# Optimization experiments

Measured on AMD Instinct MI355X. Metric: run time of the kernel, lower is better.

The kernel has to match this reference:

```python
import jax, jax.numpy as jnp
import numpy as np

RANK = 8
ALPHA = 16.0
SCALING = ALPHA / RANK
EPS = 1e-8


def setup_inputs() -> dict:
    key = jax.random.key(0)
    k1, k2, k3, k4 = jax.random.split(key, 4)
    B, S, D_IN, D_OUT = 4, 2048, 4096, 4096
    x = jax.random.normal(k1, (B, S, D_IN), dtype=jnp.float32)
    base_output = jax.random.normal(k2, (B, S, D_OUT), dtype=jnp.float32)
    base_weight = jax.random.normal(k3, (D_OUT, D_IN), dtype=jnp.float32) * 0.02
    # orthogonal init for lora_A (rank x in_features)
    g = jax.random.normal(k4, (D_IN, RANK), dtype=jnp.float32)
    q, _ = jnp.linalg.qr(g)
    lora_A = q.T.astype(jnp.float32)  # [rank, in]
    # lora_B initialized to zeros in the module; use small random values so
    # the delta path is numerically exercised.
    lora_B = jax.random.normal(jax.random.fold_in(key, 5), (D_OUT, RANK), dtype=jnp.float32) * 0.01
    magnitude = jnp.ones((D_OUT,), dtype=jnp.float32)
    return {
        "x": x,
        "base_output": base_output,
        "base_weight": base_weight,
        "lora_A": lora_A,
        "lora_B": lora_B,
        "magnitude": magnitude,
    }


def reference(x, base_output, base_weight, lora_A, lora_B, magnitude):
    # Low-rank path: x @ A^T @ B^T, scaled.  (dropout p=0 -> identity)
    lora_x = jnp.einsum("bsi,ri->bsr", x, lora_A)            # [B,S,r]
    lora_out = jnp.einsum("bsr,or->bso", lora_x, lora_B)     # [B,S,out]
    delta_v = lora_out * SCALING
    # DoRA-style row norm of the updated weight (materializes full delta,
    # matching the original math exactly).
    updated_weight = base_weight + (lora_B @ lora_A) * SCALING  # [out,in]
    updated_norm = jnp.linalg.norm(updated_weight, axis=1) + EPS  # [out]
    mag_scale = magnitude / updated_norm                          # [out]
    output = (base_output + delta_v) * mag_scale[None, None, :]
    return output
```

## Files before the change

kernel.cpp:

```cpp
#include <hip/hip_runtime.h>
#include <math.h>

#define D_IN   4096
#define D_OUT  4096
#define M_ROWS 8192
#define RANK   8
#define SCALING 2.0f
#define EPS_N  1e-8f

__global__ __launch_bounds__(256) void k_magscale(
    const float* __restrict__ W,
    const float* __restrict__ A,
    const float* __restrict__ Bl,
    const float* __restrict__ mag,
    float* __restrict__ mag_scale,
    float* __restrict__ Bm)
{
    const int wave = threadIdx.x >> 6;
    const int lane = threadIdx.x & 63;
    const int o = blockIdx.x * 4 + wave;
    const float* Wrow = W + (size_t)o * D_IN;

    float b[RANK];
#pragma unroll
    for (int r = 0; r < RANK; ++r) b[r] = Bl[o * RANK + r];

    float acc = 0.f;
    for (int i = lane * 4; i < D_IN; i += 64 * 4) {
        float4 w4 = *(const float4*)(Wrow + i);
        float dx = 0.f, dy = 0.f, dz = 0.f, dw = 0.f;
#pragma unroll
        for (int r = 0; r < RANK; ++r) {
            float4 a4 = *(const float4*)(A + r * D_IN + i);
            dx += b[r] * a4.x; dy += b[r] * a4.y;
            dz += b[r] * a4.z; dw += b[r] * a4.w;
        }
        float tx = w4.x + SCALING * dx;
        float ty = w4.y + SCALING * dy;
        float tz = w4.z + SCALING * dz;
        float tw = w4.w + SCALING * dw;
        acc += tx * tx + ty * ty + tz * tz + tw * tw;
    }
#pragma unroll
    for (int off = 32; off > 0; off >>= 1)
        acc += __shfl_down(acc, off, 64);

    if (lane == 0) {
        float ms = mag[o] / (sqrtf(acc) + EPS_N);
        mag_scale[o] = ms;
#pragma unroll
        for (int r = 0; r < RANK; ++r)
            Bm[o * RANK + r] = SCALING * b[r] * ms;
    }
}

__global__ __launch_bounds__(256) void k_lorax(
    const float* __restrict__ x,
    const float* __restrict__ A,
    float* __restrict__ lx)
{
    const int wave = threadIdx.x >> 6;
    const int lane = threadIdx.x & 63;
    const int m = blockIdx.x * 4 + wave;
    const float* xrow = x + (size_t)m * D_IN;

    float acc[RANK] = {};
    for (int i = lane * 4; i < D_IN; i += 64 * 4) {
        float4 x4 = *(const float4*)(xrow + i);
#pragma unroll
        for (int r = 0; r < RANK; ++r) {
            float4 a4 = *(const float4*)(A + r * D_IN + i);
            acc[r] += x4.x * a4.x + x4.y * a4.y + x4.z * a4.z + x4.w * a4.w;
        }
    }
#pragma unroll
    for (int r = 0; r < RANK; ++r) {
#pragma unroll
        for (int off = 32; off > 0; off >>= 1)
            acc[r] += __shfl_down(acc[r], off, 64);
    }
    if (lane == 0) {
#pragma unroll
        for (int r = 0; r < RANK; ++r)
            lx[m * RANK + r] = acc[r];
    }
}

#define MT 16
#define OT 1024

__global__ __launch_bounds__(256) void k_out(
    const float* __restrict__ base,
    const float* __restrict__ lx,
    const float* __restrict__ Bm,
    const float* __restrict__ mag_scale,
    float* __restrict__ out)
{
    const int ob = (blockIdx.x & (D_OUT / OT - 1)) * OT;
    const int mb = (blockIdx.x / (D_OUT / OT)) * MT;
    const int o = ob + threadIdx.x * 4;

    float ms[4];
    float bm[4][RANK];
#pragma unroll
    for (int j = 0; j < 4; ++j) {
        ms[j] = mag_scale[o + j];
#pragma unroll
        for (int r = 0; r < RANK; ++r)
            bm[j][r] = Bm[(size_t)(o + j) * RANK + r];
    }

    __shared__ float slx[MT][RANK];
    if (threadIdx.x < MT * RANK) {
        int mi = threadIdx.x / RANK, r = threadIdx.x % RANK;
        slx[mi][r] = lx[(size_t)(mb + mi) * RANK + r];
    }
    __syncthreads();

    for (int mi = 0; mi < MT; ++mi) {
        const size_t row = (size_t)(mb + mi) * D_OUT + o;
        float4 b4 = *(const float4*)(base + row);
        float l[RANK];
#pragma unroll
        for (int r = 0; r < RANK; ++r) l[r] = slx[mi][r];

        float rx = b4.x * ms[0];
        float ry = b4.y * ms[1];
        float rz = b4.z * ms[2];
        float rw = b4.w * ms[3];
#pragma unroll
        for (int r = 0; r < RANK; ++r) {
            rx += l[r] * bm[0][r];
            ry += l[r] * bm[1][r];
            rz += l[r] * bm[2][r];
            rw += l[r] * bm[3][r];
        }
        float4 o4 = make_float4(rx, ry, rz, rw);
        *(float4*)(out + row) = o4;
    }
}

extern "C" void kernel_launch(void* const* d_in, const int* in_sizes, int n_in,
                              void* d_out, int out_size, void* d_ws, size_t ws_size,
                              hipStream_t stream) {
    const float* x        = (const float*)d_in[0];
    const float* base_out = (const float*)d_in[1];
    const float* base_w   = (const float*)d_in[2];
    const float* lora_A   = (const float*)d_in[3];
    const float* lora_B   = (const float*)d_in[4];
    const float* mag      = (const float*)d_in[5];
    float* out = (float*)d_out;

    float* mag_scale = (float*)d_ws;
    float* Bm        = mag_scale + D_OUT;
    float* lx        = Bm + (size_t)D_OUT * RANK;

    k_magscale<<<D_OUT / 4, 256, 0, stream>>>(base_w, lora_A, lora_B, mag,
                                              mag_scale, Bm);
    k_lorax<<<M_ROWS / 4, 256, 0, stream>>>(x, lora_A, lx);
    k_out<<<(M_ROWS / MT) * (D_OUT / OT), 256, 0, stream>>>(base_out, lx, Bm,
                                                            mag_scale, out);
}
```

Baseline: 439.1 us.

## Fuse LoRA projection into output kernel and process two weight rows per wave

Merges the x·A^T projection kernel into the output kernel. Each block computes lora_x for 16 rows into shared memory and then writes all 4096 output columns for those rows, which removes one launch and the lx round trip through global memory. Each wave now handles 4 x rows and the magnitude kernel handles 2 weight rows per wave, so each load of A is reused across more rows. The cost is fewer blocks (512) with larger per-thread register use, which may limit occupancy and memory-level parallelism on the large streaming passes.

```diff
diff --git a/kernel.cpp b/kernel.cpp
--- a/kernel.cpp
+++ b/kernel.cpp
@@ -8,7 +8,7 @@
 #define SCALING 2.0f
 #define EPS_N  1e-8f
 
-__global__ __launch_bounds__(256) void k_magscale(
+__global__ __launch_bounds__(256, 2) void k_magscale(
     const float* __restrict__ W,
     const float* __restrict__ A,
     const float* __restrict__ Bl,
@@ -18,125 +18,145 @@
 {
     const int wave = threadIdx.x >> 6;
     const int lane = threadIdx.x & 63;
-    const int o = blockIdx.x * 4 + wave;
-    const float* Wrow = W + (size_t)o * D_IN;
+    const int o0 = blockIdx.x * 8 + wave * 2;
+    const float* W0 = W + (size_t)o0 * D_IN;
+    const float* W1 = W0 + D_IN;
 
-    float b[RANK];
+    float b0[RANK], b1[RANK];
 #pragma unroll
-    for (int r = 0; r < RANK; ++r) b[r] = Bl[o * RANK + r];
+    for (int r = 0; r < RANK; ++r) {
+        b0[r] = Bl[o0 * RANK + r];
+        b1[r] = Bl[(o0 + 1) * RANK + r];
+    }
 
-    float acc = 0.f;
-    for (int i = lane * 4; i < D_IN; i += 64 * 4) {
-        float4 w4 = *(const float4*)(Wrow + i);
-        float dx = 0.f, dy = 0.f, dz = 0.f, dw = 0.f;
+    float acc0 = 0.f, acc1 = 0.f;
+    for (int i = lane * 4; i < D_IN; i += 256) {
+        float4 a4[RANK];
+#pragma unroll
+        for (int r = 0; r < RANK; ++r)
+            a4[r] = *(const float4*)(A + r * D_IN + i);
+        float4 w0 = *(const float4*)(W0 + i);
+        float4 w1 = *(const float4*)(W1 + i);
+
+        float d0x = 0.f, d0y = 0.f, d0z = 0.f, d0w = 0.f;
+        float d1x = 0.f, d1y = 0.f, d1z = 0.f, d1w = 0.f;
 #pragma unroll
         for (int r = 0; r < RANK; ++r) {
-            float4 a4 = *(const float4*)(A + r * D_IN + i);
-            dx += b[r] * a4.x; dy += b[r] * a4.y;
-            dz += b[r] * a4.z; dw += b[r] * a4.w;
+            d0x += b0[r] * a4[r].x; d0y += b0[r] * a4[r].y;
+            d0z += b0[r] * a4[r].z; d0w += b0[r] * a4[r].w;
+            d1x += b1[r] * a4[r].x; d1y += b1[r] * a4[r].y;
+            d1z += b1[r] * a4[r].z; d1w += b1[r] * a4[r].w;
         }
-        float tx = w4.x + SCALING * dx;
-        float ty = w4.y + SCALING * dy;
-        float tz = w4.z + SCALING * dz;
-        float tw = w4.w + SCALING * dw;
-        acc += tx * tx + ty * ty + tz * tz + tw * tw;
+        float t;
+        t = w0.x + SCALING * d0x; acc0 += t * t;
+        t = w0.y + SCALING * d0y; acc0 += t * t;
+        t = w0.z + SCALING * d0z; acc0 += t * t;
+        t = w0.w + SCALING * d0w; acc0 += t * t;
+        t = w1.x + SCALING * d1x; acc1 += t * t;
+        t = w1.y + SCALING * d1y; acc1 += t * t;
+        t = w1.z + SCALING * d1z; acc1 += t * t;
+        t = w1.w + SCALING * d1w; acc1 += t * t;
     }
 #pragma unroll
-    for (int off = 32; off > 0; off >>= 1)
-        acc += __shfl_down(acc, off, 64);
-
+    for (int off = 32; off > 0; off >>= 1) {
+        acc0 += __shfl_down(acc0, off, 64);
+        acc1 += __shfl_down(acc1, off, 64);
+    }
     if (lane == 0) {
-        float ms = mag[o] / (sqrtf(acc) + EPS_N);
-        mag_scale[o] = ms;
-#pragma unroll
-        for (int r = 0; r < RANK; ++r)
-            Bm[o * RANK + r] = SCALING * b[r] * ms;
-    }
-}
-
-__global__ __launch_bounds__(256) void k_lorax(
-    const float* __restrict__ x,
-    const float* __restrict__ A,
-    float* __restrict__ lx)
-{
-    const int wave = threadIdx.x >> 6;
-    const int lane = threadIdx.x & 63;
-    const int m = blockIdx.x * 4 + wave;
-    const float* xrow = x + (size_t)m * D_IN;
-
-    float acc[RANK] = {};
-    for (int i = lane * 4; i < D_IN; i += 64 * 4) {
-        float4 x4 = *(const float4*)(xrow + i);
+        float ms0 = mag[o0] / (sqrtf(acc0) + EPS_N);
+        float ms1 = mag[o0 + 1] / (sqrtf(acc1) + EPS_N);
+        mag_scale[o0] = ms0;
+        mag_scale[o0 + 1] = ms1;
 #pragma unroll
         for (int r = 0; r < RANK; ++r) {
-            float4 a4 = *(const float4*)(A + r * D_IN + i);
-            acc[r] += x4.x * a4.x + x4.y * a4.y + x4.z * a4.z + x4.w * a4.w;
+            Bm[o0 * RANK + r]       = SCALING * b0[r] * ms0;
+            Bm[(o0 + 1) * RANK + r] = SCALING * b1[r] * ms1;
         }
-    }
-#pragma unroll
-    for (int r = 0; r < RANK; ++r) {
-#pragma unroll
-        for (int off = 32; off > 0; off >>= 1)
-            acc[r] += __shfl_down(acc[r], off, 64);
-    }
-    if (lane == 0) {
-#pragma unroll
-        for (int r = 0; r < RANK; ++r)
-            lx[m * RANK + r] = acc[r];
     }
 }
 
 #define MT 16
-#define OT 1024
 
-__global__ __launch_bounds__(256) void k_out(
+__global__ __launch_bounds__(256, 2) void k_fused(
+    const float* __restrict__ x,
+    const float* __restrict__ A,
     const float* __restrict__ base,
-    const float* __restrict__ lx,
     const float* __restrict__ Bm,
     const float* __restrict__ mag_scale,
     float* __restrict__ out)
 {
-    const int ob = (blockIdx.x & (D_OUT / OT - 1)) * OT;
-    const int mb = (blockIdx.x / (D_OUT / OT)) * MT;
-    const int o = ob + threadIdx.x * 4;
+    const int wave = threadIdx.x >> 6;
+    const int lane = threadIdx.x & 63;
+    const int mb = blockIdx.x * MT;
 
-    float ms[4];
-    float bm[4][RANK];
+    __shared__ float slx[MT][RANK];
+
+    const float* x0 = x + (size_t)(mb + wave * 4) * D_IN;
+    float acc[4][RANK];
 #pragma unroll
-    for (int j = 0; j < 4; ++j) {
-        ms[j] = mag_scale[o + j];
+    for (int g = 0; g < 4; ++g)
+#pragma unroll
+        for (int r = 0; r < RANK; ++r) acc[g][r] = 0.f;
+
+    for (int i = lane * 4; i < D_IN; i += 256) {
+        float4 a4[RANK];
 #pragma unroll
         for (int r = 0; r < RANK; ++r)
-            bm[j][r] = Bm[(size_t)(o + j) * RANK + r];
+            a4[r] = *(const float4*)(A + r * D_IN + i);
+#pragma unroll
+        for (int g = 0; g < 4; ++g) {
+            float4 x4 = *(const float4*)(x0 + (size_t)g * D_IN + i);
+#pragma unroll
+            for (int r = 0; r < RANK; ++r)
+                acc[g][r] += x4.x * a4[r].x + x4.y * a4[r].y +
+                             x4.z * a4[r].z + x4.w * a4[r].w;
+        }
     }
-
-    __shared__ float slx[MT][RANK];
-    if (threadIdx.x < MT * RANK) {
-        int mi = threadIdx.x / RANK, r = threadIdx.x % RANK;
-        slx[mi][r] = lx[(size_t)(mb + mi) * RANK + r];
+#pragma unroll
+    for (int g = 0; g < 4; ++g) {
+#pragma unroll
+        for (int r = 0; r < RANK; ++r) {
+            float v = acc[g][r];
+#pragma unroll
+            for (int off = 32; off > 0; off >>= 1)
+                v += __shfl_down(v, off, 64);
+            if (lane == 0) slx[wave * 4 + g][r] = v;
+        }
     }
     __syncthreads();
 
-    for (int mi = 0; mi < MT; ++mi) {
-        const size_t row = (size_t)(mb + mi) * D_OUT + o;
-        float4 b4 = *(const float4*)(base + row);
-        float l[RANK];
 #pragma unroll
-        for (int r = 0; r < RANK; ++r) l[r] = slx[mi][r];
+    for (int tile = 0; tile < 4; ++tile) {
+        const int o = tile * 1024 + threadIdx.x * 4;
+        const float4 ms4 = *(const float4*)(mag_scale + o);
+        float bm[4][RANK];
+#pragma unroll
+        for (int j = 0; j < 4; ++j) {
+            float4 lo = *(const float4*)(Bm + (size_t)(o + j) * RANK);
+            float4 hi = *(const float4*)(Bm + (size_t)(o + j) * RANK + 4);
+            bm[j][0] = lo.x; bm[j][1] = lo.y; bm[j][2] = lo.z; bm[j][3] = lo.w;
+            bm[j][4] = hi.x; bm[j][5] = hi.y; bm[j][6] = hi.z; bm[j][7] = hi.w;
+        }
+        for (int mi = 0; mi < MT; ++mi) {
+            const size_t row = (size_t)(mb + mi) * D_OUT + o;
+            float4 b4 = *(const float4*)(base + row);
+            float l[RANK];
+#pragma unroll
+            for (int r = 0; r < RANK; ++r) l[r] = slx[mi][r];
 
-        float rx = b4.x * ms[0];
-        float ry = b4.y * ms[1];
-        float rz = b4.z * ms[2];
-        float rw = b4.w * ms[3];
+            float rx = b4.x * ms4.x;
+            float ry = b4.y * ms4.y;
+            float rz = b4.z * ms4.z;
+            float rw = b4.w * ms4.w;
 #pragma unroll
-        for (int r = 0; r < RANK; ++r) {
-            rx += l[r] * bm[0][r];
-            ry += l[r] * bm[1][r];
-            rz += l[r] * bm[2][r];
-            rw += l[r] * bm[3][r];
+            for (int r = 0; r < RANK; ++r) {
+                rx += l[r] * bm[0][r];
+                ry += l[r] * bm[1][r];
+                rz += l[r] * bm[2][r];
+                rw += l[r] * bm[3][r];
+            }
+            *(float4*)(out + row) = make_float4(rx, ry, rz, rw);
         }
-        float4 o4 = make_float4(rx, ry, rz, rw);
-        *(float4*)(out + row) = o4;
     }
 }
 
@@ -153,11 +173,9 @@
 
     float* mag_scale = (float*)d_ws;
     float* Bm        = mag_scale + D_OUT;
-    float* lx        = Bm + (size_t)D_OUT * RANK;
 
-    k_magscale<<<D_OUT / 4, 256, 0, stream>>>(base_w, lora_A, lora_B, mag,
+    k_magscale<<<D_OUT / 8, 256, 0, stream>>>(base_w, lora_A, lora_B, mag,
                                               mag_scale, Bm);
-    k_lorax<<<M_ROWS / 4, 256, 0, stream>>>(x, lora_A, lx);
-    k_out<<<(M_ROWS / MT) * (D_OUT / OT), 256, 0, stream>>>(base_out, lx, Bm,
-                                                            mag_scale, out);
+    k_fused<<<M_ROWS / MT, 256, 0, stream>>>(x, lora_A, base_out, Bm,
+                                             mag_scale, out);
 }
```

Measured after the change: 415.0 us. 1.06x faster.
